# Kernel tuning notes

Measured on AMD Instinct MI355X. Metric: run time of the kernel, lower is better.

The kernel has to match this reference:

```python
import jax, jax.numpy as jnp
import numpy as np

IN_FEATURES = 1024
OUT_FEATURES = 1024
N_LEAF = 16
BATCH = 4096


def setup_inputs() -> dict:
    key = jax.random.key(0)
    k_x, k_gw, k_pw = jax.random.split(key, 3)
    x = jax.random.normal(k_x, (BATCH, IN_FEATURES), dtype=jnp.float32)
    # xavier_normal for gating weights [in, L]
    gw_std = np.sqrt(2.0 / (IN_FEATURES + N_LEAF))
    gw = jax.random.normal(k_gw, (IN_FEATURES, N_LEAF), dtype=jnp.float32) * gw_std
    gb = jnp.zeros((N_LEAF,), dtype=jnp.float32)
    # kaiming_normal (linear) on [out*L, in] then reshaped to [out, in, L]
    pw_std = np.sqrt(1.0 / IN_FEATURES)
    pw = jax.random.normal(k_pw, (OUT_FEATURES, IN_FEATURES, N_LEAF), dtype=jnp.float32) * pw_std
    pb = jnp.zeros((OUT_FEATURES, N_LEAF), dtype=jnp.float32)
    return {"x": x, "gw": gw, "gb": gb, "pw": pw, "pb": pb}


def reference(x, gw, gb, pw, pb):
    # gatings: softmax over leaves, [B, L]
    g = jax.nn.softmax(x @ gw + gb, axis=1)
    # Fused contraction order (same math as materializing per-sample [out,in]
    # projection matrices): per-leaf projections then gating-weighted sum.
    # leaf_out[b,o,l] = sum_i x[b,i] * pw[o,i,l]
    leaf_out = jnp.einsum('bi,oil->bol', x, pw)
    # result[b,o] = sum_l leaf_out[b,o,l] * g[b,l] + sum_l pb[o,l] * g[b,l]
    result = jnp.einsum('bol,bl->bo', leaf_out, g) + g @ pb.T
    return result
```

## Files before the change

### kernel.cpp

```cpp
#include <hip/hip_runtime.h>
#include <hip/hip_bf16.h>
#include <stdint.h>

#define IN_F   1024
#define OUT_F  1024
#define NLEAF  16
#define BATCH  4096

#define KK      1024
#define NN      (OUT_F * NLEAF)
#define BM      256
#define BN      256
#define BK      32
#define NKT     (KK / BK)
#define ABYTES  (BM * BK * 2)
#define SLICE   (2 * ABYTES)
#define GS_PAD  257

typedef __bf16 bf16x8 __attribute__((ext_vector_type(8)));
typedef float  f32x4  __attribute__((ext_vector_type(4)));

#define ASYNC_COPY16(gp, lp)                                                         \
  __builtin_amdgcn_global_load_lds((const __attribute__((address_space(1))) void*)(gp), \
                                   (__attribute__((address_space(3))) void*)(lp),       \
                                   16, 0, 0)

__global__ __launch_bounds__(256) void prep_kernel(
    const float* __restrict__ x, const float* __restrict__ gw,
    const float* __restrict__ gb, const float* __restrict__ pw,
    float* __restrict__ g, __hip_bfloat16* __restrict__ xb,
    __hip_bfloat16* __restrict__ W) {
  __shared__ __align__(16) __hip_bfloat16 lt[16 * 264];
  const int t = threadIdx.x;

  if (blockIdx.x < OUT_F) {
    const int o = blockIdx.x;
    const float* src = pw + (size_t)o * (IN_F * NLEAF);
    for (int ch = 0; ch < 4; ++ch) {
      const float4* p = (const float4*)(src + ch * 4096 + t * 16);
      const float4 v0 = p[0], v1 = p[1], v2 = p[2], v3 = p[3];
      if (ch) __syncthreads();
      lt[ 0 * 264 + t] = __float2bfloat16(v0.x);
      lt[ 1 * 264 + t] = __float2bfloat16(v0.y);
      lt[ 2 * 264 + t] = __float2bfloat16(v0.z);
      lt[ 3 * 264 + t] = __float2bfloat16(v0.w);
      lt[ 4 * 264 + t] = __float2bfloat16(v1.x);
      lt[ 5 * 264 + t] = __float2bfloat16(v1.y);
      lt[ 6 * 264 + t] = __float2bfloat16(v1.z);
      lt[ 7 * 264 + t] = __float2bfloat16(v1.w);
      lt[ 8 * 264 + t] = __float2bfloat16(v2.x);
      lt[ 9 * 264 + t] = __float2bfloat16(v2.y);
      lt[10 * 264 + t] = __float2bfloat16(v2.z);
      lt[11 * 264 + t] = __float2bfloat16(v2.w);
      lt[12 * 264 + t] = __float2bfloat16(v3.x);
      lt[13 * 264 + t] = __float2bfloat16(v3.y);
      lt[14 * 264 + t] = __float2bfloat16(v3.z);
      lt[15 * 264 + t] = __float2bfloat16(v3.w);
      __syncthreads();
#pragma unroll
      for (int jj = 0; jj < 2; ++jj) {
        const int u = t + 256 * jj;
        const int l = u >> 5;
        const int i8 = (u & 31) * 8;
        *(uint4*)(W + ((size_t)o * NLEAF + l) * KK + ch * 256 + i8) =
            *(const uint4*)(lt + l * 264 + i8);
      }
    }
  } else {
    const int blk  = blockIdx.x - OUT_F;
    const int lane = t & 63;
    const int wv   = t >> 6;
    const int b    = blk * 4 + wv;
    const int i4   = lane >> 4;
    const int l    = lane & 15;

    const float* xrow = x + (size_t)b * IN_F;
    float acc = 0.f;
#pragma unroll 8
    for (int k = 0; k < IN_F / 4; ++k) {
      const float xv = xrow[k * 4 + i4];
      const float wvv = gw[k * 64 + lane];
      acc = fmaf(xv, wvv, acc);
    }
    acc += __shfl_xor(acc, 16);
    acc += __shfl_xor(acc, 32);
    float logit = acc + gb[l];
    float m = logit;
#pragma unroll
    for (int off = 8; off > 0; off >>= 1) m = fmaxf(m, __shfl_xor(m, off));
    float e = __expf(logit - m);
    float s = e;
#pragma unroll
    for (int off = 8; off > 0; off >>= 1) s += __shfl_xor(s, off);
    if (lane < NLEAF) g[b * NLEAF + l] = e / s;

    const float* xblk = x + (size_t)blk * 4 * IN_F;
    __hip_bfloat16* xbblk = xb + (size_t)blk * 4 * IN_F;
#pragma unroll
    for (int j = 0; j < 2; ++j) {
      const int f = (t + 256 * j) * 8;
      const float4 a0 = *(const float4*)(xblk + f);
      const float4 a1 = *(const float4*)(xblk + f + 4);
      __align__(16) __hip_bfloat16 tmp[8];
      tmp[0] = __float2bfloat16(a0.x); tmp[1] = __float2bfloat16(a0.y);
      tmp[2] = __float2bfloat16(a0.z); tmp[3] = __float2bfloat16(a0.w);
      tmp[4] = __float2bfloat16(a1.x); tmp[5] = __float2bfloat16(a1.y);
      tmp[6] = __float2bfloat16(a1.z); tmp[7] = __float2bfloat16(a1.w);
      *(uint4*)(xbblk + f) = *(const uint4*)tmp;
    }
  }
}

#define STAGE_A(tt)                                                  \
  do {                                                               \
    char* _d = smem + (((tt) & 3) * SLICE);                          \
    const __hip_bfloat16* _s = aG + (long)(tt) * BK;                 \
    ASYNC_COPY16(_s + gOff0, _d + c0 * 16);                          \
    ASYNC_COPY16(_s + gOff1, _d + c1 * 16);                          \
  } while (0)

#define STAGE_B(tt)                                                  \
  do {                                                               \
    char* _d = smem + (((tt) & 3) * SLICE) + ABYTES;                 \
    const __hip_bfloat16* _s = bG + (long)(tt) * BK;                 \
    ASYNC_COPY16(_s + gOff0, _d + c0 * 16);                          \
    ASYNC_COPY16(_s + gOff1, _d + c1 * 16);                          \
  } while (0)

#define TILE_ITER(tt, DO_STAGE, TAILVM)                                        \
  do {                                                                         \
    const __hip_bfloat16* As =                                                 \
        (const __hip_bfloat16*)(smem + ((tt) & 3) * SLICE);                    \
    const __hip_bfloat16* Bs =                                                 \
        (const __hip_bfloat16*)(smem + ((tt) & 3) * SLICE + ABYTES);           \
    bf16x8 af0, af1, af2, af3, bv0, bv1, bv2, bv3;                             \
    af0 = *(const bf16x8*)(As + ((wr * 128 +  0 + r16) * 4 + (quad ^ swz)) * 8); \
    af1 = *(const bf16x8*)(As + ((wr * 128 + 16 + r16) * 4 + (quad ^ swz)) * 8); \
    af2 = *(const bf16x8*)(As + ((wr * 128 + 32 + r16) * 4 + (quad ^ swz)) * 8); \
    af3 = *(const bf16x8*)(As + ((wr * 128 + 48 + r16) * 4 + (quad ^ swz)) * 8); \
    bv0 = *(const bf16x8*)(Bs + ((wc * 64 +  0 + r16) * 4 + (quad ^ swz)) * 8);  \
    bv1 = *(const bf16x8*)(Bs + ((wc * 64 + 16 + r16) * 4 + (quad ^ swz)) * 8);  \
    bv2 = *(const bf16x8*)(Bs + ((wc * 64 + 32 + r16) * 4 + (quad ^ swz)) * 8);  \
    bv3 = *(const bf16x8*)(Bs + ((wc * 64 + 48 + r16) * 4 + (quad ^ swz)) * 8);  \
    if (DO_STAGE) STAGE_A((tt) + 3);                                           \
    __builtin_amdgcn_s_barrier();                                              \
    asm volatile("s_waitcnt lgkmcnt(0)" ::: "memory");                         \
    __builtin_amdgcn_sched_barrier(0);                                         \
    __builtin_amdgcn_s_setprio(1);                                             \
    acc[0][0] = __builtin_amdgcn_mfma_f32_16x16x32_bf16(af0, bv0, acc[0][0], 0, 0, 0); \
    acc[0][1] = __builtin_amdgcn_mfma_f32_16x16x32_bf16(af0, bv1, acc[0][1], 0, 0, 0); \
    acc[0][2] = __builtin_amdgcn_mfma_f32_16x16x32_bf16(af0, bv2, acc[0][2], 0, 0, 0); \
    acc[0][3] = __builtin_amdgcn_mfma_f32_16x16x32_bf16(af0, bv3, acc[0][3], 0, 0, 0); \
    acc[1][0] = __builtin_amdgcn_mfma_f32_16x16x32_bf16(af1, bv0, acc[1][0], 0, 0, 0); \
    acc[1][1] = __builtin_amdgcn_mfma_f32_16x16x32_bf16(af1, bv1, acc[1][1], 0, 0, 0); \
    acc[1][2] = __builtin_amdgcn_mfma_f32_16x16x32_bf16(af1, bv2, acc[1][2], 0, 0, 0); \
    acc[1][3] = __builtin_amdgcn_mfma_f32_16x16x32_bf16(af1, bv3, acc[1][3], 0, 0, 0); \
    acc[2][0] = __builtin_amdgcn_mfma_f32_16x16x32_bf16(af2, bv0, acc[2][0], 0, 0, 0); \
    acc[2][1] = __builtin_amdgcn_mfma_f32_16x16x32_bf16(af2, bv1, acc[2][1], 0, 0, 0); \
    acc[2][2] = __builtin_amdgcn_mfma_f32_16x16x32_bf16(af2, bv2, acc[2][2], 0, 0, 0); \
    acc[2][3] = __builtin_amdgcn_mfma_f32_16x16x32_bf16(af2, bv3, acc[2][3], 0, 0, 0); \
    acc[3][0] = __builtin_amdgcn_mfma_f32_16x16x32_bf16(af3, bv0, acc[3][0], 0, 0, 0); \
    acc[3][1] = __builtin_amdgcn_mfma_f32_16x16x32_bf16(af3, bv1, acc[3][1], 0, 0, 0); \
    acc[3][2] = __builtin_amdgcn_mfma_f32_16x16x32_bf16(af3, bv2, acc[3][2], 0, 0, 0); \
    acc[3][3] = __builtin_amdgcn_mfma_f32_16x16x32_bf16(af3, bv3, acc[3][3], 0, 0, 0); \
    __builtin_amdgcn_s_setprio(0);                                             \
    __builtin_amdgcn_s_barrier();                                              \
    af0 = *(const bf16x8*)(As + ((wr * 128 +  64 + r16) * 4 + (quad ^ swz)) * 8); \
    af1 = *(const bf16x8*)(As + ((wr * 128 +  80 + r16) * 4 + (quad ^ swz)) * 8); \
    af2 = *(const bf16x8*)(As + ((wr * 128 +  96 + r16) * 4 + (quad ^ swz)) * 8); \
    af3 = *(const bf16x8*)(As + ((wr * 128 + 112 + r16) * 4 + (quad ^ swz)) * 8); \
    if (DO_STAGE) STAGE_B((tt) + 3);                                           \
    TAILVM;                                                                    \
    __builtin_amdgcn_s_barrier();                                              \
    asm volatile("s_waitcnt lgkmcnt(0)" ::: "memory");                         \
    __builtin_amdgcn_sched_barrier(0);                                         \
    __builtin_amdgcn_s_setprio(1);                                             \
    acc[4][0] = __builtin_amdgcn_mfma_f32_16x16x32_bf16(af0, bv0, acc[4][0], 0, 0, 0); \
    acc[4][1] = __builtin_amdgcn_mfma_f32_16x16x32_bf16(af0, bv1, acc[4][1], 0, 0, 0); \
    acc[4][2] = __builtin_amdgcn_mfma_f32_16x16x32_bf16(af0, bv2, acc[4][2], 0, 0, 0); \
    acc[4][3] = __builtin_amdgcn_mfma_f32_16x16x32_bf16(af0, bv3, acc[4][3], 0, 0, 0); \
    acc[5][0] = __builtin_amdgcn_mfma_f32_16x16x32_bf16(af1, bv0, acc[5][0], 0, 0, 0); \
    acc[5][1] = __builtin_amdgcn_mfma_f32_16x16x32_bf16(af1, bv1, acc[5][1], 0, 0, 0); \
    acc[5][2] = __builtin_amdgcn_mfma_f32_16x16x32_bf16(af1, bv2, acc[5][2], 0, 0, 0); \
    acc[5][3] = __builtin_amdgcn_mfma_f32_16x16x32_bf16(af1, bv3, acc[5][3], 0, 0, 0); \
    acc[6][0] = __builtin_amdgcn_mfma_f32_16x16x32_bf16(af2, bv0, acc[6][0], 0, 0, 0); \
    acc[6][1] = __builtin_amdgcn_mfma_f32_16x16x32_bf16(af2, bv1, acc[6][1], 0, 0, 0); \
    acc[6][2] = __builtin_amdgcn_mfma_f32_16x16x32_bf16(af2, bv2, acc[6][2], 0, 0, 0); \
    acc[6][3] = __builtin_amdgcn_mfma_f32_16x16x32_bf16(af2, bv3, acc[6][3], 0, 0, 0); \
    acc[7][0] = __builtin_amdgcn_mfma_f32_16x16x32_bf16(af3, bv0, acc[7][0], 0, 0, 0); \
    acc[7][1] = __builtin_amdgcn_mfma_f32_16x16x32_bf16(af3, bv1, acc[7][1], 0, 0, 0); \
    acc[7][2] = __builtin_amdgcn_mfma_f32_16x16x32_bf16(af3, bv2, acc[7][2], 0, 0, 0); \
    acc[7][3] = __builtin_amdgcn_mfma_f32_16x16x32_bf16(af3, bv3, acc[7][3], 0, 0, 0); \
    __builtin_amdgcn_s_setprio(0);                                             \
    __builtin_amdgcn_s_barrier();                                              \
  } while (0)

__global__ __launch_bounds__(512, 2) void gemm_kernel(
    const __hip_bfloat16* __restrict__ Xb,
    const __hip_bfloat16* __restrict__ W,
    const float* __restrict__ g,
    const float* __restrict__ pb,
    float* __restrict__ out) {
  extern __shared__ __align__(16) char smem[];

  const int t    = threadIdx.x;
  const int lane = t & 63;
  const int w    = t >> 6;
  const int quad = lane >> 4;
  const int r16  = lane & 15;
  const int wr   = w >> 2;
  const int wc   = w & 3;
  const int swz  = (r16 >> 1) & 3;

  const int b0 = blockIdx.x * BN;
  const int n0 = blockIdx.y * BM;

  const __hip_bfloat16* aG = W  + (long)n0 * KK;
  const __hip_bfloat16* bG = Xb + (long)b0 * KK;

  const int  c0 = t, c1 = t + 512;
  const long gOff0 = (long)(c0 >> 2) * KK + (long)(((c0 & 3) ^ ((c0 >> 3) & 3)) * 8);
  const long gOff1 = (long)(c1 >> 2) * KK + (long)(((c1 & 3) ^ ((c1 >> 3) & 3)) * 8);

  f32x4 acc[8][4] = {};

  STAGE_A(0); STAGE_B(0);
  STAGE_A(1); STAGE_B(1);
  STAGE_A(2); STAGE_B(2);
  asm volatile("s_waitcnt vmcnt(8)" ::: "memory");
  __builtin_amdgcn_s_barrier();

  for (int tt = 0; tt < NKT - 3; ++tt)
    TILE_ITER(tt, 1, asm volatile("s_waitcnt vmcnt(8)" ::: "memory"));
  TILE_ITER(NKT - 3, 0, asm volatile("s_waitcnt vmcnt(4)" ::: "memory"));
  TILE_ITER(NKT - 2, 0, asm volatile("s_waitcnt vmcnt(0)" ::: "memory"));
  TILE_ITER(NKT - 1, 0, (void)0);

  float* gs  = (float*)smem;
  float* pbs = (float*)(smem + 16 * GS_PAD * 4);
#pragma unroll
  for (int j = 0; j < 8; ++j) {
    const int f = t + 512 * j;
    gs[(f & 15) * GS_PAD + (f >> 4)] = g[b0 * NLEAF + f];
  }
  if (t < 256) pbs[t] = pb[(n0 >> 4) * NLEAF + t];
  __syncthreads();

  const int oBase = (n0 >> 4) + wr * 8;
#pragma unroll
  for (int ni = 0; ni < 4; ++ni) {
    const int bl = wc * 64 + ni * 16 + r16;
    float gv[4];
#pragma unroll
    for (int r = 0; r < 4; ++r) gv[r] = gs[(quad * 4 + r) * GS_PAD + bl];
    float rv[8];
#pragma unroll
    for (int mi = 0; mi < 8; ++mi) {
      float v = 0.f;
#pragma unroll
      for (int r = 0; r < 4; ++r)
        v = fmaf(acc[mi][ni][r] + pbs[(wr * 8 + mi) * NLEAF + quad * 4 + r],
                 gv[r], v);
      v += __shfl_xor(v, 16);
      v += __shfl_xor(v, 32);
      rv[mi] = v;
    }
    if (quad == 0) {
      *(float4*)(out + (long)(b0 + bl) * OUT_F + oBase) =
          make_float4(rv[0], rv[1], rv[2], rv[3]);
      *(float4*)(out + (long)(b0 + bl) * OUT_F + oBase + 4) =
          make_float4(rv[4], rv[5], rv[6], rv[7]);
    }
  }
}

__global__ __launch_bounds__(256) void gate_kernel_fb(
    const float* __restrict__ x, const float* __restrict__ gw,
    const float* __restrict__ gb, float* __restrict__ g) {
  const int lane = threadIdx.x & 63;
  const int wv   = threadIdx.x >> 6;
  const int b    = blockIdx.x * 4 + wv;
  const int i4   = lane >> 4;
  const int l    = lane & 15;
  const float* xrow = x + (size_t)b * IN_F;
  float acc = 0.f;
  for (int k = 0; k < IN_F / 4; ++k)
    acc = fmaf(xrow[k * 4 + i4], gw[k * 64 + lane], acc);
  acc += __shfl_xor(acc, 16);
  acc += __shfl_xor(acc, 32);
  float logit = acc + gb[l];
  float m = logit;
  for (int off = 8; off > 0; off >>= 1) m = fmaxf(m, __shfl_xor(m, off));
  float e = __expf(logit - m);
  float s = e;
  for (int off = 8; off > 0; off >>= 1) s += __shfl_xor(s, off);
  if (lane < NLEAF) g[b * NLEAF + l] = e / s;
}

__global__ __launch_bounds__(256) void fallback_kernel(
    const float* __restrict__ x, const float* __restrict__ pw,
    const float* __restrict__ pb, const float* __restrict__ g,
    float* __restrict__ out) {
  const int b = blockIdx.x;
  __shared__ float xs[IN_F];
  __shared__ float gsl[NLEAF];
  const int t = threadIdx.x;
  for (int j = t; j < IN_F; j += 256) xs[j] = x[(long)b * IN_F + j];
  if (t < NLEAF) gsl[t] = g[b * NLEAF + t];
  __syncthreads();
  for (int o = t; o < OUT_F; o += 256) {
    const float* pwo = pw + (long)o * (IN_F * NLEAF);
    float acc = 0.f;
    for (int i = 0; i < IN_F; ++i) {
      const float xv = xs[i];
      float wsum = 0.f;
#pragma unroll
      for (int l = 0; l < NLEAF; ++l) wsum += gsl[l] * pwo[i * NLEAF + l];
      acc += xv * wsum;
    }
    float bias = 0.f;
#pragma unroll
    for (int l = 0; l < NLEAF; ++l) bias += gsl[l] * pb[o * NLEAF + l];
    out[(long)b * OUT_F + o] = acc + bias;
  }
}

extern "C" void kernel_launch(void* const* d_in, const int* in_sizes, int n_in,
                              void* d_out, int out_size, void* d_ws, size_t ws_size,
                              hipStream_t stream) {
  const float* x  = (const float*)d_in[0];
  const float* gw = (const float*)d_in[1];
  const float* gb = (const float*)d_in[2];
  const float* pw = (const float*)d_in[3];
  const float* pb = (const float*)d_in[4];
  float* out = (float*)d_out;

  const size_t w_bytes  = (size_t)NN * KK * sizeof(__hip_bfloat16);
  const size_t xb_bytes = (size_t)BATCH * KK * sizeof(__hip_bfloat16);
  const size_t g_bytes  = (size_t)BATCH * NLEAF * sizeof(float);

  if (ws_size >= w_bytes + xb_bytes + g_bytes) {
    __hip_bfloat16* W  = (__hip_bfloat16*)d_ws;
    __hip_bfloat16* xb = (__hip_bfloat16*)((char*)d_ws + w_bytes);
    float*          g  = (float*)((char*)d_ws + w_bytes + xb_bytes);

    static int attr_done = 0;
    if (!attr_done) {
      (void)hipFuncSetAttribute((const void*)gemm_kernel,
                                hipFuncAttributeMaxDynamicSharedMemorySize,
                                4 * SLICE);
      attr_done = 1;
    }

    prep_kernel<<<OUT_F + BATCH / 4, 256, 0, stream>>>(x, gw, gb, pw, g, xb, W);
    gemm_kernel<<<dim3(BATCH / BN, NN / BM), 512, 4 * SLICE, stream>>>(
        xb, W, g, pb, out);
  } else {
    float* g = (float*)d_ws;
    gate_kernel_fb<<<BATCH / 4, 256, 0, stream>>>(x, gw, gb, g);
    fallback_kernel<<<BATCH, 256, 0, stream>>>(x, pw, pb, g, out);
  }
}
```

Measured before the change: 259.4 us.

## Cut GEMM barriers to one per K-tile, unroll ring slots, split prep kernel

New measurement: 261.8 us. No clear change (+0.9%).

```diff
diff --git a/kernel.cpp b/kernel.cpp
--- a/kernel.cpp
+++ b/kernel.cpp
@@ -25,114 +25,98 @@
                                    (__attribute__((address_space(3))) void*)(lp),       \
                                    16, 0, 0)
 
-__global__ __launch_bounds__(256) void prep_kernel(
+#define VM8  asm volatile("s_waitcnt vmcnt(8)" ::: "memory")
+#define VM4  asm volatile("s_waitcnt vmcnt(4)" ::: "memory")
+#define VM0  asm volatile("s_waitcnt vmcnt(0)" ::: "memory")
+#define NOVM ((void)0)
+
+__global__ __launch_bounds__(256) void prep_w_kernel(
+    const float* __restrict__ pw, __hip_bfloat16* __restrict__ W) {
+  const int o  = blockIdx.x;
+  const int t  = threadIdx.x;
+  const int l  = t & 15;
+  const int ic = t >> 4;
+  const float* src = pw + (size_t)o * (IN_F * NLEAF) + l;
+  __hip_bfloat16* dst = W + ((size_t)o * NLEAF + l) * KK;
+#pragma unroll
+  for (int ib = 0; ib < 8; ++ib) {
+    const int i0 = ib * 128 + ic * 8;
+    float v[8];
+#pragma unroll
+    for (int j = 0; j < 8; ++j) v[j] = src[(size_t)(i0 + j) * NLEAF];
+    __align__(16) __hip_bfloat16 tmp[8];
+#pragma unroll
+    for (int j = 0; j < 8; ++j) tmp[j] = __float2bfloat16(v[j]);
+    *(uint4*)(dst + i0) = *(const uint4*)tmp;
+  }
+}
+
+__global__ __launch_bounds__(256) void prep_x_kernel(
     const float* __restrict__ x, const float* __restrict__ gw,
-    const float* __restrict__ gb, const float* __restrict__ pw,
-    float* __restrict__ g, __hip_bfloat16* __restrict__ xb,
-    __hip_bfloat16* __restrict__ W) {
-  __shared__ __align__(16) __hip_bfloat16 lt[16 * 264];
-  const int t = threadIdx.x;
-
-  if (blockIdx.x < OUT_F) {
-    const int o = blockIdx.x;
-    const float* src = pw + (size_t)o * (IN_F * NLEAF);
-    for (int ch = 0; ch < 4; ++ch) {
-      const float4* p = (const float4*)(src + ch * 4096 + t * 16);
-      const float4 v0 = p[0], v1 = p[1], v2 = p[2], v3 = p[3];
-      if (ch) __syncthreads();
-      lt[ 0 * 264 + t] = __float2bfloat16(v0.x);
-      lt[ 1 * 264 + t] = __float2bfloat16(v0.y);
-      lt[ 2 * 264 + t] = __float2bfloat16(v0.z);
-      lt[ 3 * 264 + t] = __float2bfloat16(v0.w);
-      lt[ 4 * 264 + t] = __float2bfloat16(v1.x);
-      lt[ 5 * 264 + t] = __float2bfloat16(v1.y);
-      lt[ 6 * 264 + t] = __float2bfloat16(v1.z);
-      lt[ 7 * 264 + t] = __float2bfloat16(v1.w);
-      lt[ 8 * 264 + t] = __float2bfloat16(v2.x);
-      lt[ 9 * 264 + t] = __float2bfloat16(v2.y);
-      lt[10 * 264 + t] = __float2bfloat16(v2.z);
-      lt[11 * 264 + t] = __float2bfloat16(v2.w);
-      lt[12 * 264 + t] = __float2bfloat16(v3.x);
-      lt[13 * 264 + t] = __float2bfloat16(v3.y);
-      lt[14 * 264 + t] = __float2bfloat16(v3.z);
-      lt[15 * 264 + t] = __float2bfloat16(v3.w);
-      __syncthreads();
-#pragma unroll
-      for (int jj = 0; jj < 2; ++jj) {
-        const int u = t + 256 * jj;
-        const int l = u >> 5;
-        const int i8 = (u & 31) * 8;
-        *(uint4*)(W + ((size_t)o * NLEAF + l) * KK + ch * 256 + i8) =
-            *(const uint4*)(lt + l * 264 + i8);
-      }
-    }
-  } else {
-    const int blk  = blockIdx.x - OUT_F;
-    const int lane = t & 63;
-    const int wv   = t >> 6;
-    const int b    = blk * 4 + wv;
-    const int i4   = lane >> 4;
-    const int l    = lane & 15;
-
-    const float* xrow = x + (size_t)b * IN_F;
-    float acc = 0.f;
+    const float* __restrict__ gb, float* __restrict__ g,
+    __hip_bfloat16* __restrict__ xb) {
+  const int t    = threadIdx.x;
+  const int blk  = blockIdx.x;
+  const int lane = t & 63;
+  const int wv   = t >> 6;
+  const int b    = blk * 4 + wv;
+  const int i4   = lane >> 4;
+  const int l    = lane & 15;
+
+  const float* xrow = x + (size_t)b * IN_F;
+  float acc = 0.f;
 #pragma unroll 8
-    for (int k = 0; k < IN_F / 4; ++k) {
-      const float xv = xrow[k * 4 + i4];
-      const float wvv = gw[k * 64 + lane];
-      acc = fmaf(xv, wvv, acc);
-    }
-    acc += __shfl_xor(acc, 16);
-    acc += __shfl_xor(acc, 32);
-    float logit = acc + gb[l];
-    float m = logit;
-#pragma unroll
-    for (int off = 8; off > 0; off >>= 1) m = fmaxf(m, __shfl_xor(m, off));
-    float e = __expf(logit - m);
-    float s = e;
-#pragma unroll
-    for (int off = 8; off > 0; off >>= 1) s += __shfl_xor(s, off);
-    if (lane < NLEAF) g[b * NLEAF + l] = e / s;
-
-    const float* xblk = x + (size_t)blk * 4 * IN_F;
-    __hip_bfloat16* xbblk = xb + (size_t)blk * 4 * IN_F;
-#pragma unroll
-    for (int j = 0; j < 2; ++j) {
-      const int f = (t + 256 * j) * 8;
-      const float4 a0 = *(const float4*)(xblk + f);
-      const float4 a1 = *(const float4*)(xblk + f + 4);
-      __align__(16) __hip_bfloat16 tmp[8];
-      tmp[0] = __float2bfloat16(a0.x); tmp[1] = __float2bfloat16(a0.y);
-      tmp[2] = __float2bfloat16(a0.z); tmp[3] = __float2bfloat16(a0.w);
-      tmp[4] = __float2bfloat16(a1.x); tmp[5] = __float2bfloat16(a1.y);
-      tmp[6] = __float2bfloat16(a1.z); tmp[7] = __float2bfloat16(a1.w);
-      *(uint4*)(xbblk + f) = *(const uint4*)tmp;
-    }
-  }
-}
-
-#define STAGE_A(tt)                                                  \
+  for (int k = 0; k < IN_F / 4; ++k) {
+    const float xv = xrow[k * 4 + i4];
+    const float wvv = gw[k * 64 + lane];
+    acc = fmaf(xv, wvv, acc);
+  }
+  acc += __shfl_xor(acc, 16);
+  acc += __shfl_xor(acc, 32);
+  float logit = acc + gb[l];
+  float m = logit;
+#pragma unroll
+  for (int off = 8; off > 0; off >>= 1) m = fmaxf(m, __shfl_xor(m, off));
+  float e = __expf(logit - m);
+  float s = e;
+#pragma unroll
+  for (int off = 8; off > 0; off >>= 1) s += __shfl_xor(s, off);
+  if (lane < NLEAF) g[b * NLEAF + l] = e / s;
+
+  const float* xblk = x + (size_t)blk * 4 * IN_F;
+  __hip_bfloat16* xbblk = xb + (size_t)blk * 4 * IN_F;
+#pragma unroll
+  for (int j = 0; j < 2; ++j) {
+    const int f = (t + 256 * j) * 8;
+    const float4 a0 = *(const float4*)(xblk + f);
+    const float4 a1 = *(const float4*)(xblk + f + 4);
+    __align__(16) __hip_bfloat16 tmp[8];
+    tmp[0] = __float2bfloat16(a0.x); tmp[1] = __float2bfloat16(a0.y);
+    tmp[2] = __float2bfloat16(a0.z); tmp[3] = __float2bfloat16(a0.w);
+    tmp[4] = __float2bfloat16(a1.x); tmp[5] = __float2bfloat16(a1.y);
+    tmp[6] = __float2bfloat16(a1.z); tmp[7] = __float2bfloat16(a1.w);
+    *(uint4*)(xbblk + f) = *(const uint4*)tmp;
+  }
+}
+
+#define STAGE_AB(tt, SL3)                                            \
   do {                                                               \
-    char* _d = smem + (((tt) & 3) * SLICE);                          \
-    const __hip_bfloat16* _s = aG + (long)(tt) * BK;                 \
-    ASYNC_COPY16(_s + gOff0, _d + c0 * 16);                          \
-    ASYNC_COPY16(_s + gOff1, _d + c1 * 16);                          \
+    char* _dA = smem + (SL3) * SLICE;                                \
+    char* _dB = _dA + ABYTES;                                        \
+    const __hip_bfloat16* _sA = aG + (long)(tt) * BK;                \
+    const __hip_bfloat16* _sB = bG + (long)(tt) * BK;                \
+    ASYNC_COPY16(_sA + gOff0, _dA + c0 * 16);                        \
+    ASYNC_COPY16(_sA + gOff1, _dA + c1 * 16);                        \
+    ASYNC_COPY16(_sB + gOff0, _dB + c0 * 16);                        \
+    ASYNC_COPY16(_sB + gOff1, _dB + c1 * 16);                        \
   } while (0)
 
-#define STAGE_B(tt)                                                  \
-  do {                                                               \
-    char* _d = smem + (((tt) & 3) * SLICE) + ABYTES;                 \
-    const __hip_bfloat16* _s = bG + (long)(tt) * BK;                 \
-    ASYNC_COPY16(_s + gOff0, _d + c0 * 16);                          \
-    ASYNC_COPY16(_s + gOff1, _d + c1 * 16);                          \
-  } while (0)
-
-#define TILE_ITER(tt, DO_STAGE, TAILVM)                                        \
+#define TILE_ITER(tt, SL, DO_STAGE, TAILVM)                                    \
   do {                                                                         \
     const __hip_bfloat16* As =                                                 \
-        (const __hip_bfloat16*)(smem + ((tt) & 3) * SLICE);                    \
+        (const __hip_bfloat16*)(smem + (SL) * SLICE);                          \
     const __hip_bfloat16* Bs =                                                 \
-        (const __hip_bfloat16*)(smem + ((tt) & 3) * SLICE + ABYTES);           \
+        (const __hip_bfloat16*)(smem + (SL) * SLICE + ABYTES);                 \
     bf16x8 af0, af1, af2, af3, bv0, bv1, bv2, bv3;                             \
     af0 = *(const bf16x8*)(As + ((wr * 128 +  0 + r16) * 4 + (quad ^ swz)) * 8); \
     af1 = *(const bf16x8*)(As + ((wr * 128 + 16 + r16) * 4 + (quad ^ swz)) * 8); \
@@ -142,8 +126,7 @@
     bv1 = *(const bf16x8*)(Bs + ((wc * 64 + 16 + r16) * 4 + (quad ^ swz)) * 8);  \
     bv2 = *(const bf16x8*)(Bs + ((wc * 64 + 32 + r16) * 4 + (quad ^ swz)) * 8);  \
     bv3 = *(const bf16x8*)(Bs + ((wc * 64 + 48 + r16) * 4 + (quad ^ swz)) * 8);  \
-    if (DO_STAGE) STAGE_A((tt) + 3);                                           \
-    __builtin_amdgcn_s_barrier();                                              \
+    if (DO_STAGE) STAGE_AB((tt) + 3, ((SL) + 3) & 3);                          \
     asm volatile("s_waitcnt lgkmcnt(0)" ::: "memory");                         \
     __builtin_amdgcn_sched_barrier(0);                                         \
     __builtin_amdgcn_s_setprio(1);                                             \
@@ -164,14 +147,10 @@
     acc[3][2] = __builtin_amdgcn_mfma_f32_16x16x32_bf16(af3, bv2, acc[3][2], 0, 0, 0); \
     acc[3][3] = __builtin_amdgcn_mfma_f32_16x16x32_bf16(af3, bv3, acc[3][3], 0, 0, 0); \
     __builtin_amdgcn_s_setprio(0);                                             \
-    __builtin_amdgcn_s_barrier();                                              \
     af0 = *(const bf16x8*)(As + ((wr * 128 +  64 + r16) * 4 + (quad ^ swz)) * 8); \
     af1 = *(const bf16x8*)(As + ((wr * 128 +  80 + r16) * 4 + (quad ^ swz)) * 8); \
     af2 = *(const bf16x8*)(As + ((wr * 128 +  96 + r16) * 4 + (quad ^ swz)) * 8); \
     af3 = *(const bf16x8*)(As + ((wr * 128 + 112 + r16) * 4 + (quad ^ swz)) * 8); \
-    if (DO_STAGE) STAGE_B((tt) + 3);                                           \
-    TAILVM;                                                                    \
-    __builtin_amdgcn_s_barrier();                                              \
     asm volatile("s_waitcnt lgkmcnt(0)" ::: "memory");                         \
     __builtin_amdgcn_sched_barrier(0);                                         \
     __builtin_amdgcn_s_setprio(1);                                             \
@@ -192,6 +171,7 @@
     acc[7][2] = __builtin_amdgcn_mfma_f32_16x16x32_bf16(af3, bv2, acc[7][2], 0, 0, 0); \
     acc[7][3] = __builtin_amdgcn_mfma_f32_16x16x32_bf16(af3, bv3, acc[7][3], 0, 0, 0); \
     __builtin_amdgcn_s_setprio(0);                                             \
+    TAILVM;                                                                    \
     __builtin_amdgcn_s_barrier();                                              \
   } while (0)
 
@@ -224,17 +204,20 @@
 
   f32x4 acc[8][4] = {};
 
-  STAGE_A(0); STAGE_B(0);
-  STAGE_A(1); STAGE_B(1);
-  STAGE_A(2); STAGE_B(2);
-  asm volatile("s_waitcnt vmcnt(8)" ::: "memory");
+  STAGE_AB(0, 0); STAGE_AB(1, 1); STAGE_AB(2, 2);
+  VM8;
   __builtin_amdgcn_s_barrier();
 
-  for (int tt = 0; tt < NKT - 3; ++tt)
-    TILE_ITER(tt, 1, asm volatile("s_waitcnt vmcnt(8)" ::: "memory"));
-  TILE_ITER(NKT - 3, 0, asm volatile("s_waitcnt vmcnt(4)" ::: "memory"));
-  TILE_ITER(NKT - 2, 0, asm volatile("s_waitcnt vmcnt(0)" ::: "memory"));
-  TILE_ITER(NKT - 1, 0, (void)0);
+  for (int tb = 0; tb < NKT - 4; tb += 4) {
+    TILE_ITER(tb + 0, 0, 1, VM8);
+    TILE_ITER(tb + 1, 1, 1, VM8);
+    TILE_ITER(tb + 2, 2, 1, VM8);
+    TILE_ITER(tb + 3, 3, 1, VM8);
+  }
+  TILE_ITER(NKT - 4, 0, 1, VM8);
+  TILE_ITER(NKT - 3, 1, 0, VM4);
+  TILE_ITER(NKT - 2, 2, 0, VM0);
+  TILE_ITER(NKT - 1, 3, 0, NOVM);
 
   float* gs  = (float*)smem;
   float* pbs = (float*)(smem + 16 * GS_PAD * 4);
@@ -352,7 +335,8 @@
       attr_done = 1;
     }
 
-    prep_kernel<<<OUT_F + BATCH / 4, 256, 0, stream>>>(x, gw, gb, pw, g, xb, W);
+    prep_w_kernel<<<OUT_F, 256, 0, stream>>>(pw, W);
+    prep_x_kernel<<<BATCH / 4, 256, 0, stream>>>(x, gw, gb, g, xb);
     gemm_kernel<<<dim3(BATCH / BN, NN / BM), 512, 4 * SLICE, stream>>>(
         xb, W, g, pb, out);
   } else {
```
